# Optimization experiments

Measured on AMD Instinct MI355X. Metric: run time of the kernel, lower is better.

Reference implementation:

```python
import jax, jax.numpy as jnp
import numpy as np

EMBED_DIM = 1024
HEAD_SIZE = 64
BATCH = 8
SEQ = 2048


def setup_inputs() -> dict:
    key = jax.random.key(0)
    k1, k2, k3, k4 = jax.random.split(key, 4)
    x = jax.random.normal(k1, (BATCH, SEQ, EMBED_DIM), dtype=jnp.float32)
    # Dense(use_bias=False) kernels: [in, out]
    scale = 1.0 / np.sqrt(EMBED_DIM)
    Wq = jax.random.normal(k2, (EMBED_DIM, HEAD_SIZE), dtype=jnp.float32) * scale
    Wk = jax.random.normal(k3, (EMBED_DIM, HEAD_SIZE), dtype=jnp.float32) * scale
    Wv = jax.random.normal(k4, (EMBED_DIM, HEAD_SIZE), dtype=jnp.float32) * scale
    return {"x": x, "Wq": Wq, "Wk": Wk, "Wv": Wv}


def reference(x, Wq, Wk, Wv):
    B, S, E = x.shape
    q = jnp.einsum("bse,eh->bsh", x, Wq)
    k = jnp.einsum("bse,eh->bsh", x, Wk)
    v = jnp.einsum("bse,eh->bsh", x, Wv)
    # scores scaled by embedding_dim**-0.5 (as in the original code)
    w = jnp.einsum("bqh,bkh->bqk", q, k) * (E ** -0.5)
    causal = jnp.tril(jnp.ones((S, S), dtype=bool))  # True on/below diag
    w = jnp.where(causal, w, -jnp.inf)
    w = jax.nn.softmax(w, axis=-1)
    # dropout is identity at inference
    return jnp.einsum("bqk,bkh->bqh", w, v)
```

## Files before the change

kernel.cpp:

```cpp
#include <hip/hip_runtime.h>
#include <hip/hip_bf16.h>


#define BATCH 8
#define SEQ   2048
#define EMB   1024
#define HD    64
#define ROWS  (BATCH*SEQ)
#define NTOT  192
#define BK    64
#define NKT   (EMB / BK)

typedef __attribute__((ext_vector_type(8))) short short8;
typedef __attribute__((ext_vector_type(4))) float floatx4;

static __device__ __forceinline__ short f2bf(float f) {
  union { __hip_bfloat16 h; short s; } u;
  u.h = __float2bfloat16(f);
  return u.s;
}

static __device__ __forceinline__ short8 pack8(float4 u, float4 v) {
  short8 r;
  r[0] = f2bf(u.x); r[1] = f2bf(u.y); r[2] = f2bf(u.z); r[3] = f2bf(u.w);
  r[4] = f2bf(v.x); r[5] = f2bf(v.y); r[6] = f2bf(v.z); r[7] = f2bf(v.w);
  return r;
}

static __device__ __forceinline__ void gload_lds16(const void* g, void* l) {
  __builtin_amdgcn_global_load_lds(
      (const __attribute__((address_space(1))) unsigned int*)g,
      (__attribute__((address_space(3))) unsigned int*)l, 16, 0, 0);
}

__global__ __launch_bounds__(256) void wt_kernel(
    const float* __restrict__ Wq, const float* __restrict__ Wk,
    const float* __restrict__ Wv, short* __restrict__ Wd) {
  const int id = blockIdx.x * 256 + threadIdx.x;
  const int lane = id & 63;
  const int ks = (id >> 6) & 1;
  const int id2 = id >> 7;
  const int nt = id2 % 12;
  const int kt = id2 / 12;
  const int lo = lane & 15, quad = lane >> 4;
  const int np = nt * 16 + lo;
  const float* __restrict__ W = (np < 64) ? Wq : ((np < 128) ? Wk : Wv);
  const int n = np & 63;
  const int k0 = kt * BK + (4 * ks + quad) * 8;
  short8 o;
#pragma unroll
  for (int u = 0; u < 8; ++u) o[u] = f2bf(W[(size_t)(k0 + u) * HD + n]);
  *(short8*)(Wd + (size_t)id * 8) = o;
}

__global__ __launch_bounds__(256, 2) void proj_kernel(
    const float* __restrict__ x, const short* __restrict__ Wd,
    short* __restrict__ qb, short* __restrict__ kb_, short* __restrict__ vtb) {
  __shared__ __align__(16) float As[2][32 * 64];

  const int t = threadIdx.x, lane = t & 63, w = t >> 6;
  const int lo = lane & 15, quad = lane >> 4;
  const int e = lo & 7;
  const int m0 = blockIdx.x * 32;

  const int cc0 = w * 2, cc1 = cc0 + 1;
  const int ar0 = cc0 * 4 + quad;
  const int ar1 = cc1 * 4 + quad;
  const float* agp0 = x + (size_t)(m0 + ar0) * EMB + ((lo ^ (ar0 & 7)) * 4);
  const float* agp1 = x + (size_t)(m0 + ar1) * EMB + ((lo ^ (ar1 & 7)) * 4);

  const short* bgp = Wd + (size_t)(w * 3) * 1024 + lane * 8;

  floatx4 acc[2][3];
#pragma unroll
  for (int mf = 0; mf < 2; ++mf)
#pragma unroll
    for (int j = 0; j < 3; ++j) acc[mf][j] = (floatx4){0.f, 0.f, 0.f, 0.f};

  short8 bcur[3][2], bnxt[3][2];

  auto STAGE_A = [&](int buf, int kt) {
    gload_lds16(agp0 + kt * BK, &As[buf][cc0 * 256]);
    gload_lds16(agp1 + kt * BK, &As[buf][cc1 * 256]);
  };
  auto LOAD_B = [&](short8 (&bf)[3][2], int kt) {
    const short* bg = bgp + (size_t)kt * 12288;
#pragma unroll
    for (int j = 0; j < 3; ++j)
#pragma unroll
      for (int ks = 0; ks < 2; ++ks)
        bf[j][ks] = *(const short8*)(bg + j * 1024 + ks * 512);
  };

  STAGE_A(0, 0);
  LOAD_B(bcur, 0);
  int buf = 0;
#pragma unroll
  for (int kt = 0; kt < NKT; ++kt) {
    __syncthreads();
    if (kt + 1 < NKT) {
      STAGE_A(buf ^ 1, kt + 1);
      LOAD_B(bnxt, kt + 1);
    }
    short8 af[2][2];
#pragma unroll
    for (int mf = 0; mf < 2; ++mf) {
      const float* Ar = &As[buf][(mf * 16 + lo) * 64];
#pragma unroll
      for (int ks = 0; ks < 2; ++ks) {
        const float4 f0 = *(const float4*)(Ar + (((8 * ks + 2 * quad) ^ e) << 2));
        const float4 f1 = *(const float4*)(Ar + (((8 * ks + 2 * quad + 1) ^ e) << 2));
        af[mf][ks] = pack8(f0, f1);
      }
    }
#pragma unroll
    for (int ks = 0; ks < 2; ++ks)
#pragma unroll
      for (int j = 0; j < 3; ++j) {
        acc[0][j] = __builtin_amdgcn_mfma_f32_16x16x32_bf16(af[0][ks], bcur[j][ks], acc[0][j], 0, 0, 0);
        acc[1][j] = __builtin_amdgcn_mfma_f32_16x16x32_bf16(af[1][ks], bcur[j][ks], acc[1][j], 0, 0, 0);
      }
#pragma unroll
    for (int j = 0; j < 3; ++j)
#pragma unroll
      for (int ks = 0; ks < 2; ++ks) bcur[j][ks] = bnxt[j][ks];
    buf ^= 1;
  }

  const int bb = m0 >> 11;
  const int sbase = (m0 & (SEQ - 1)) + quad * 4;
#pragma unroll
  for (int mf = 0; mf < 2; ++mf) {
    const int rowb = m0 + mf * 16 + quad * 4;
#pragma unroll
    for (int j = 0; j < 3; ++j) {
      const int nt = w * 3 + j;
      const floatx4 v = acc[mf][j];
      if (nt < 4) {
#pragma unroll
        for (int r = 0; r < 4; ++r)
          qb[(size_t)(rowb + r) * HD + nt * 16 + lo] = f2bf(v[r] * 0.03125f);
      } else if (nt < 8) {
#pragma unroll
        for (int r = 0; r < 4; ++r)
          kb_[(size_t)(rowb + r) * HD + (nt - 4) * 16 + lo] = f2bf(v[r]);
      } else {
        const int col = (nt - 8) * 16 + lo;
        short4 sv = make_short4(f2bf(v[0]), f2bf(v[1]), f2bf(v[2]), f2bf(v[3]));
        *(short4*)(vtb + ((size_t)bb * HD + col) * SEQ + sbase + mf * 16) = sv;
      }
    }
  }
}

#define PSTR 40

__global__ __launch_bounds__(256, 2) void attn_kernel(
    const short* __restrict__ qb, const short* __restrict__ kb,
    const short* __restrict__ vtb, float* __restrict__ out) {
  __shared__ __align__(16) short Ps[4][16 * PSTR];
  __shared__ __align__(16) floatx4 Red[2][5][64];

  const int b = blockIdx.y;
  const int bx = blockIdx.x;
  const int qx = (bx & 1) ? (63 - (bx >> 1)) : (bx >> 1);
  const int q0 = qx * 32;
  const int t = threadIdx.x, lane = t & 63, w = t >> 6;
  const int wr = w >> 1, wk = w & 1;
  const int lo = lane & 15, quad = lane >> 4;

  const short* qp = qb + ((size_t)b * SEQ + q0 + wr * 16 + lo) * HD + quad * 8;
  const short8 qf0 = *(const short8*)(qp);
  const short8 qf1 = *(const short8*)(qp + 32);

  const short* __restrict__ kgb = kb + (size_t)b * SEQ * HD;
  const short* __restrict__ vgb = vtb + (size_t)b * HD * SEQ;
  const short* kbase = kgb + (size_t)(wk * 32 + lo) * HD + quad * 8;
  const short* vbase = vgb + (size_t)lo * SEQ + wk * 32 + quad * 8;

  floatx4 acc[4];
  float lsum[4] = {0.f, 0.f, 0.f, 0.f};
#pragma unroll
  for (int nt = 0; nt < 4; ++nt) acc[nt] = (floatx4){0.f, 0.f, 0.f, 0.f};

  auto LOAD = [&](short8 (&kf)[2][2], short8 (&vf)[4], int j0) {
    const short* kp = kbase + (size_t)j0 * HD;
#pragma unroll
    for (int n2 = 0; n2 < 2; ++n2) {
      kf[n2][0] = *(const short8*)(kp + n2 * (16 * HD));
      kf[n2][1] = *(const short8*)(kp + n2 * (16 * HD) + 32);
    }
    const short* vp = vbase + j0;
#pragma unroll
    for (int nt = 0; nt < 4; ++nt)
      vf[nt] = *(const short8*)(vp + (size_t)(nt * 16) * SEQ);
  };

  short* Pw = Ps[w];
  const int rowb = q0 + wr * 16 + quad * 4;

  auto STEP = [&](short8 (&kf)[2][2], short8 (&vf)[4], int j0) {
    floatx4 s0 = (floatx4){0.f, 0.f, 0.f, 0.f};
    floatx4 s1 = (floatx4){0.f, 0.f, 0.f, 0.f};
    __builtin_amdgcn_s_setprio(1);
    s0 = __builtin_amdgcn_mfma_f32_16x16x32_bf16(qf0, kf[0][0], s0, 0, 0, 0);
    s0 = __builtin_amdgcn_mfma_f32_16x16x32_bf16(qf1, kf[0][1], s0, 0, 0, 0);
    s1 = __builtin_amdgcn_mfma_f32_16x16x32_bf16(qf0, kf[1][0], s1, 0, 0, 0);
    s1 = __builtin_amdgcn_mfma_f32_16x16x32_bf16(qf1, kf[1][1], s1, 0, 0, 0);
    __builtin_amdgcn_s_setprio(0);

    const bool diag = (j0 + 64 > q0);
#pragma unroll
    for (int r = 0; r < 4; ++r) {
      float e0 = __expf(s0[r]);
      float e1 = __expf(s1[r]);
      if (diag) {
        const int key0 = j0 + wk * 32 + lo;
        e0 = (key0 <= rowb + r) ? e0 : 0.f;
        e1 = (key0 + 16 <= rowb + r) ? e1 : 0.f;
      }
      lsum[r] += e0 + e1;
      Pw[(quad * 4 + r) * PSTR + lo] = f2bf(e0);
      Pw[(quad * 4 + r) * PSTR + 16 + lo] = f2bf(e1);
    }
    const short8 pf = *(const short8*)(&Pw[lo * PSTR + quad * 8]);
    __builtin_amdgcn_s_setprio(1);
#pragma unroll
    for (int nt = 0; nt < 4; ++nt)
      acc[nt] = __builtin_amdgcn_mfma_f32_16x16x32_bf16(pf, vf[nt], acc[nt], 0, 0, 0);
    __builtin_amdgcn_s_setprio(0);
  };

  const int niter = q0 / 64 + 1;
  short8 kA[2][2], vA[4], kB[2][2], vB[4];
  LOAD(kA, vA, 0);
  int it = 0;
  while (true) {
    if (it + 1 < niter) LOAD(kB, vB, (it + 1) * 64);
    STEP(kA, vA, it * 64);
    ++it; if (it >= niter) break;
    if (it + 1 < niter) LOAD(kA, vA, (it + 1) * 64);
    STEP(kB, vB, it * 64);
    ++it; if (it >= niter) break;
  }

#pragma unroll
  for (int d = 1; d < 16; d <<= 1) {
#pragma unroll
    for (int r = 0; r < 4; ++r) lsum[r] += __shfl_xor(lsum[r], d);
  }

  if (wk == 1) {
#pragma unroll
    for (int nt = 0; nt < 4; ++nt) Red[wr][nt][lane] = acc[nt];
    Red[wr][4][lane] = (floatx4){lsum[0], lsum[1], lsum[2], lsum[3]};
  }
  __syncthreads();
  if (wk == 0) {
    const floatx4 lp = Red[wr][4][lane];
    float invd[4];
#pragma unroll
    for (int r = 0; r < 4; ++r) invd[r] = 1.0f / (lsum[r] + lp[r]);
#pragma unroll
    for (int nt = 0; nt < 4; ++nt) {
      const floatx4 o = acc[nt] + Red[wr][nt][lane];
#pragma unroll
      for (int r = 0; r < 4; ++r)
        out[((size_t)b * SEQ + rowb + r) * HD + nt * 16 + lo] = o[r] * invd[r];
    }
  }
}

extern "C" void kernel_launch(void* const* d_in, const int* in_sizes, int n_in,
                              void* d_out, int out_size, void* d_ws, size_t ws_size,
                              hipStream_t stream) {
  const float* x  = (const float*)d_in[0];
  const float* Wq = (const float*)d_in[1];
  const float* Wk = (const float*)d_in[2];
  const float* Wv = (const float*)d_in[3];
  float* out = (float*)d_out;
  short* ws = (short*)d_ws;
  short* qbp = ws;
  short* kbp = ws + (size_t)ROWS * HD;
  short* vtp = ws + (size_t)2 * ROWS * HD;
  short* Wd  = ws + (size_t)3 * ROWS * HD;

  wt_kernel<<<dim3(96), 256, 0, stream>>>(Wq, Wk, Wv, Wd);
  proj_kernel<<<dim3(ROWS / 32), 256, 0, stream>>>(x, Wd, qbp, kbp, vtp);
  attn_kernel<<<dim3(SEQ / 32, BATCH), 256, 0, stream>>>(qbp, kbp, vtp, out);
}
```

Before: 175.6 us.

## Split attention over key ranges, add combine kernel, stage bf16 A via registers

The attention kernel now splits each query tile's causal key range into four chunks across separate blocks, writing partial numerators and denominators that a new combine kernel sums and normalizes. This targets load imbalance and low occupancy from the triangular work distribution, and occupancy hints are raised. The projection kernel now loads x through registers, converts it to bf16 before storing to shared memory, and drops the direct global-to-LDS loads. The attention inner loop loses its explicit double-buffered prefetch. The split adds an extra kernel launch and extra global traffic for the partial results.

```diff
diff --git a/kernel.cpp b/kernel.cpp
--- a/kernel.cpp
+++ b/kernel.cpp
@@ -7,9 +7,9 @@
 #define EMB   1024
 #define HD    64
 #define ROWS  (BATCH*SEQ)
-#define NTOT  192
 #define BK    64
 #define NKT   (EMB / BK)
+#define NSPLIT 4
 
 typedef __attribute__((ext_vector_type(8))) short short8;
 typedef __attribute__((ext_vector_type(4))) float floatx4;
@@ -25,12 +25,6 @@
   r[0] = f2bf(u.x); r[1] = f2bf(u.y); r[2] = f2bf(u.z); r[3] = f2bf(u.w);
   r[4] = f2bf(v.x); r[5] = f2bf(v.y); r[6] = f2bf(v.z); r[7] = f2bf(v.w);
   return r;
-}
-
-static __device__ __forceinline__ void gload_lds16(const void* g, void* l) {
-  __builtin_amdgcn_global_load_lds(
-      (const __attribute__((address_space(1))) unsigned int*)g,
-      (__attribute__((address_space(3))) unsigned int*)l, 16, 0, 0);
 }
 
 __global__ __launch_bounds__(256) void wt_kernel(
@@ -56,18 +50,16 @@
 __global__ __launch_bounds__(256, 2) void proj_kernel(
     const float* __restrict__ x, const short* __restrict__ Wd,
     short* __restrict__ qb, short* __restrict__ kb_, short* __restrict__ vtb) {
-  __shared__ __align__(16) float As[2][32 * 64];
+  __shared__ __align__(16) short Ab[2][32 * 64];
 
   const int t = threadIdx.x, lane = t & 63, w = t >> 6;
   const int lo = lane & 15, quad = lane >> 4;
   const int e = lo & 7;
   const int m0 = blockIdx.x * 32;
 
-  const int cc0 = w * 2, cc1 = cc0 + 1;
-  const int ar0 = cc0 * 4 + quad;
-  const int ar1 = cc1 * 4 + quad;
-  const float* agp0 = x + (size_t)(m0 + ar0) * EMB + ((lo ^ (ar0 & 7)) * 4);
-  const float* agp1 = x + (size_t)(m0 + ar1) * EMB + ((lo ^ (ar1 & 7)) * 4);
+  const int srow = t >> 3, sc = t & 7;
+  const float* sgp = x + (size_t)(m0 + srow) * EMB + sc * 8;
+  const int sslot = srow * 64 + ((sc ^ (srow & 7)) << 3);
 
   const short* bgp = Wd + (size_t)(w * 3) * 1024 + lane * 8;
 
@@ -78,10 +70,12 @@
     for (int j = 0; j < 3; ++j) acc[mf][j] = (floatx4){0.f, 0.f, 0.f, 0.f};
 
   short8 bcur[3][2], bnxt[3][2];
-
-  auto STAGE_A = [&](int buf, int kt) {
-    gload_lds16(agp0 + kt * BK, &As[buf][cc0 * 256]);
-    gload_lds16(agp1 + kt * BK, &As[buf][cc1 * 256]);
+  float4 ra, rb;
+
+  auto LOADA = [&](int kt) {
+    const float* p = sgp + kt * BK;
+    ra = *(const float4*)(p);
+    rb = *(const float4*)(p + 4);
   };
   auto LOAD_B = [&](short8 (&bf)[3][2], int kt) {
     const short* bg = bgp + (size_t)kt * 12288;
@@ -92,27 +86,22 @@
         bf[j][ks] = *(const short8*)(bg + j * 1024 + ks * 512);
   };
 
-  STAGE_A(0, 0);
+  LOADA(0);
   LOAD_B(bcur, 0);
+  *(short8*)(&Ab[0][sslot]) = pack8(ra, rb);
+  __syncthreads();
+
   int buf = 0;
-#pragma unroll
   for (int kt = 0; kt < NKT; ++kt) {
-    __syncthreads();
-    if (kt + 1 < NKT) {
-      STAGE_A(buf ^ 1, kt + 1);
-      LOAD_B(bnxt, kt + 1);
-    }
+    const bool more = (kt + 1 < NKT);
+    if (more) { LOADA(kt + 1); LOAD_B(bnxt, kt + 1); }
     short8 af[2][2];
 #pragma unroll
-    for (int mf = 0; mf < 2; ++mf) {
-      const float* Ar = &As[buf][(mf * 16 + lo) * 64];
-#pragma unroll
-      for (int ks = 0; ks < 2; ++ks) {
-        const float4 f0 = *(const float4*)(Ar + (((8 * ks + 2 * quad) ^ e) << 2));
-        const float4 f1 = *(const float4*)(Ar + (((8 * ks + 2 * quad + 1) ^ e) << 2));
-        af[mf][ks] = pack8(f0, f1);
-      }
-    }
+    for (int mf = 0; mf < 2; ++mf)
+#pragma unroll
+      for (int ks = 0; ks < 2; ++ks)
+        af[mf][ks] = *(const short8*)(
+            &Ab[buf][(mf * 16 + lo) * 64 + (((4 * ks + quad) ^ e) << 3)]);
 #pragma unroll
     for (int ks = 0; ks < 2; ++ks)
 #pragma unroll
@@ -120,10 +109,14 @@
         acc[0][j] = __builtin_amdgcn_mfma_f32_16x16x32_bf16(af[0][ks], bcur[j][ks], acc[0][j], 0, 0, 0);
         acc[1][j] = __builtin_amdgcn_mfma_f32_16x16x32_bf16(af[1][ks], bcur[j][ks], acc[1][j], 0, 0, 0);
       }
-#pragma unroll
-    for (int j = 0; j < 3; ++j)
-#pragma unroll
-      for (int ks = 0; ks < 2; ++ks) bcur[j][ks] = bnxt[j][ks];
+    if (more) {
+      *(short8*)(&Ab[buf ^ 1][sslot]) = pack8(ra, rb);
+#pragma unroll
+      for (int j = 0; j < 3; ++j)
+#pragma unroll
+        for (int ks = 0; ks < 2; ++ks) bcur[j][ks] = bnxt[j][ks];
+    }
+    __syncthreads();
     buf ^= 1;
   }
 
@@ -155,20 +148,26 @@
 
 #define PSTR 40
 
-__global__ __launch_bounds__(256, 2) void attn_kernel(
+__global__ __launch_bounds__(256, 6) void attn_kernel(
     const short* __restrict__ qb, const short* __restrict__ kb,
-    const short* __restrict__ vtb, float* __restrict__ out) {
+    const short* __restrict__ vtb, float* __restrict__ pacc,
+    float* __restrict__ plsum) {
   __shared__ __align__(16) short Ps[4][16 * PSTR];
   __shared__ __align__(16) floatx4 Red[2][5][64];
 
   const int b = blockIdx.y;
   const int bx = blockIdx.x;
-  const int qx = (bx & 1) ? (63 - (bx >> 1)) : (bx >> 1);
+  const int qx = bx >> 2;
+  const int sp = bx & 3;
   const int q0 = qx * 32;
   const int t = threadIdx.x, lane = t & 63, w = t >> 6;
   const int wr = w >> 1, wk = w & 1;
   const int lo = lane & 15, quad = lane >> 4;
 
+  const int niter = q0 / 64 + 1;
+  const int it0 = (sp * niter) >> 2;
+  const int it1 = ((sp + 1) * niter) >> 2;
+
   const short* qp = qb + ((size_t)b * SEQ + q0 + wr * 16 + lo) * HD + quad * 8;
   const short8 qf0 = *(const short8*)(qp);
   const short8 qf1 = *(const short8*)(qp + 32);
@@ -183,23 +182,25 @@
 #pragma unroll
   for (int nt = 0; nt < 4; ++nt) acc[nt] = (floatx4){0.f, 0.f, 0.f, 0.f};
 
-  auto LOAD = [&](short8 (&kf)[2][2], short8 (&vf)[4], int j0) {
-    const short* kp = kbase + (size_t)j0 * HD;
-#pragma unroll
-    for (int n2 = 0; n2 < 2; ++n2) {
-      kf[n2][0] = *(const short8*)(kp + n2 * (16 * HD));
-      kf[n2][1] = *(const short8*)(kp + n2 * (16 * HD) + 32);
-    }
-    const short* vp = vbase + j0;
-#pragma unroll
-    for (int nt = 0; nt < 4; ++nt)
-      vf[nt] = *(const short8*)(vp + (size_t)(nt * 16) * SEQ);
-  };
-
   short* Pw = Ps[w];
   const int rowb = q0 + wr * 16 + quad * 4;
 
-  auto STEP = [&](short8 (&kf)[2][2], short8 (&vf)[4], int j0) {
+  for (int it = it0; it < it1; ++it) {
+    const int j0 = it * 64;
+    short8 kf[2][2], vf[4];
+    {
+      const short* kp = kbase + (size_t)j0 * HD;
+#pragma unroll
+      for (int n2 = 0; n2 < 2; ++n2) {
+        kf[n2][0] = *(const short8*)(kp + n2 * (16 * HD));
+        kf[n2][1] = *(const short8*)(kp + n2 * (16 * HD) + 32);
+      }
+      const short* vp = vbase + j0;
+#pragma unroll
+      for (int nt = 0; nt < 4; ++nt)
+        vf[nt] = *(const short8*)(vp + (size_t)(nt * 16) * SEQ);
+    }
+
     floatx4 s0 = (floatx4){0.f, 0.f, 0.f, 0.f};
     floatx4 s1 = (floatx4){0.f, 0.f, 0.f, 0.f};
     __builtin_amdgcn_s_setprio(1);
@@ -229,19 +230,6 @@
     for (int nt = 0; nt < 4; ++nt)
       acc[nt] = __builtin_amdgcn_mfma_f32_16x16x32_bf16(pf, vf[nt], acc[nt], 0, 0, 0);
     __builtin_amdgcn_s_setprio(0);
-  };
-
-  const int niter = q0 / 64 + 1;
-  short8 kA[2][2], vA[4], kB[2][2], vB[4];
-  LOAD(kA, vA, 0);
-  int it = 0;
-  while (true) {
-    if (it + 1 < niter) LOAD(kB, vB, (it + 1) * 64);
-    STEP(kA, vA, it * 64);
-    ++it; if (it >= niter) break;
-    if (it + 1 < niter) LOAD(kA, vA, (it + 1) * 64);
-    STEP(kB, vB, it * 64);
-    ++it; if (it >= niter) break;
   }
 
 #pragma unroll
@@ -258,17 +246,39 @@
   __syncthreads();
   if (wk == 0) {
     const floatx4 lp = Red[wr][4][lane];
-    float invd[4];
-#pragma unroll
-    for (int r = 0; r < 4; ++r) invd[r] = 1.0f / (lsum[r] + lp[r]);
 #pragma unroll
     for (int nt = 0; nt < 4; ++nt) {
       const floatx4 o = acc[nt] + Red[wr][nt][lane];
 #pragma unroll
       for (int r = 0; r < 4; ++r)
-        out[((size_t)b * SEQ + rowb + r) * HD + nt * 16 + lo] = o[r] * invd[r];
-    }
-  }
+        pacc[(((size_t)b * SEQ + rowb + r) * NSPLIT + sp) * HD + nt * 16 + lo] = o[r];
+    }
+    if (lo == 0) {
+#pragma unroll
+      for (int r = 0; r < 4; ++r)
+        plsum[((size_t)b * SEQ + rowb + r) * NSPLIT + sp] = lsum[r] + lp[r];
+    }
+  }
+}
+
+__global__ __launch_bounds__(256) void comb_kernel(
+    const float* __restrict__ pacc, const float* __restrict__ plsum,
+    float* __restrict__ out) {
+  const int idx = blockIdx.x * 256 + threadIdx.x;
+  const int row = idx >> 4;
+  const int h4 = (idx & 15) << 2;
+  const float* pa = pacc + (size_t)row * (NSPLIT * HD) + h4;
+  float4 s = make_float4(0.f, 0.f, 0.f, 0.f);
+  float d = 0.f;
+#pragma unroll
+  for (int sp = 0; sp < NSPLIT; ++sp) {
+    const float4 v = *(const float4*)(pa + sp * HD);
+    s.x += v.x; s.y += v.y; s.z += v.z; s.w += v.w;
+    d += plsum[(size_t)row * NSPLIT + sp];
+  }
+  const float inv = 1.0f / d;
+  float4 o = make_float4(s.x * inv, s.y * inv, s.z * inv, s.w * inv);
+  *(float4*)(out + (size_t)row * HD + h4) = o;
 }
 
 extern "C" void kernel_launch(void* const* d_in, const int* in_sizes, int n_in,
@@ -284,8 +294,11 @@
   short* kbp = ws + (size_t)ROWS * HD;
   short* vtp = ws + (size_t)2 * ROWS * HD;
   short* Wd  = ws + (size_t)3 * ROWS * HD;
+  float* pacc  = (float*)(ws + (size_t)3 * ROWS * HD + 196608);
+  float* plsum = pacc + (size_t)ROWS * NSPLIT * HD;
 
   wt_kernel<<<dim3(96), 256, 0, stream>>>(Wq, Wk, Wv, Wd);
   proj_kernel<<<dim3(ROWS / 32), 256, 0, stream>>>(x, Wd, qbp, kbp, vtp);
-  attn_kernel<<<dim3(SEQ / 32, BATCH), 256, 0, stream>>>(qbp, kbp, vtp, out);
-}
+  attn_kernel<<<dim3(64 * NSPLIT, BATCH), 256, 0, stream>>>(qbp, kbp, vtp, pacc, plsum);
+  comb_kernel<<<dim3(ROWS * 16 / 256), 256, 0, stream>>>(pacc, plsum, out);
+}
```

New measurement: 163.2 us. -7.0%, faster.
